# Optimization experiments

Measured on AMD Instinct MI355X. Metric: run time of the kernel, lower is better.

The kernel has to match this reference:

```python
import jax, jax.numpy as jnp
import numpy as np

N_NODES = 20000
N_EDGES = 640000
D = 128            # node feature dim
NUM_HEADS = 4      # = num_irreps of edge_sh (lmax=3, 0e+1o+2e+3o)
HEAD_DIM = D // NUM_HEADS
IR_DIMS = np.array([1, 3, 5, 7])  # dims of each irrep; sum = 16
AVG_NUM_NEIGHBORS = 32.0


def setup_inputs() -> dict:
    key = jax.random.key(0)
    ks = jax.random.split(key, 20)
    inp = {
        "edge_sh": jax.random.normal(ks[0], (N_EDGES, int(IR_DIMS.sum())), jnp.float32),
        "node_feats": jax.random.normal(ks[1], (N_NODES, D), jnp.float32),
        "edge_feats": jax.random.normal(ks[2], (N_EDGES, 64), jnp.float32),
        "chi_scalar": jax.random.normal(ks[3], (N_EDGES, 64), jnp.float32),
        "cutoffs": jax.random.uniform(ks[4], (N_EDGES,), jnp.float32),
        "senders": jax.random.randint(ks[5], (N_EDGES,), 0, N_NODES),
        "receivers": jax.random.randint(ks[6], (N_EDGES,), 0, N_NODES),
        # radial MLP: 64 -> 128 -> 128 (silu between)
        "W_rad1": jax.random.normal(ks[7], (64, 128), jnp.float32) / np.sqrt(64),
        "b_rad1": jnp.zeros((128,), jnp.float32),
        "W_rad2": jax.random.normal(ks[8], (128, 128), jnp.float32) / np.sqrt(128),
        "b_rad2": jnp.zeros((128,), jnp.float32),
        # spherical-scalar MLP: 64 -> 128 -> 128
        "W_sph1": jax.random.normal(ks[9], (64, 128), jnp.float32) / np.sqrt(64),
        "b_sph1": jnp.zeros((128,), jnp.float32),
        "W_sph2": jax.random.normal(ks[10], (128, 128), jnp.float32) / np.sqrt(128),
        "b_sph2": jnp.zeros((128,), jnp.float32),
        # Q/K projections, no bias
        "Wq": jax.random.normal(ks[11], (D, D), jnp.float32) / np.sqrt(D),
        "Wk": jax.random.normal(ks[12], (D, D), jnp.float32) / np.sqrt(D),
    }
    return inp


def reference(edge_sh, node_feats, edge_feats, chi_scalar, cutoffs, senders,
              receivers, W_rad1, b_rad1, W_rad2, b_rad2, W_sph1, b_sph1,
              W_sph2, b_sph2, Wq, Wk):
    silu = jax.nn.silu
    # edge filter: radial MLP + spherical-scalar MLP
    w = silu(edge_feats @ W_rad1 + b_rad1) @ W_rad2 + b_rad2      # [E, D]
    w = w + (silu(chi_scalar @ W_sph1 + b_sph1) @ W_sph2 + b_sph2)
    w = w.reshape(-1, NUM_HEADS, HEAD_DIM)                        # [E, H, hd]
    # gathered queries/keys
    q = (node_feats @ Wq).reshape(-1, NUM_HEADS, HEAD_DIM)[receivers]
    k = (node_feats @ Wk).reshape(-1, NUM_HEADS, HEAD_DIM)[senders]
    # filter-scaled attention: per-edge, per-head scalar
    alpha = (q * w * k).sum(axis=-1) * (1.0 / np.sqrt(HEAD_DIM))  # [E, H]
    alpha = alpha * cutoffs[:, None]
    # aligned_mul: broadcast per-irrep weight over each irrep's dim (mul=1)
    y = jnp.repeat(alpha, IR_DIMS, axis=-1)                       # [E, 16]
    msg = edge_sh * y
    # scatter_sum into receivers
    chi = jax.ops.segment_sum(msg, receivers, num_segments=N_NODES)
    return chi / AVG_NUM_NEIGHBORS
```

## Files before the change

### kernel.cpp

```cpp
#include <hip/hip_runtime.h>
#include <cmath>

#define NNODES 20000
#define NEDGES 640000
#define DDIM   128
#define TN     16
#define BE     64

typedef __attribute__((ext_vector_type(8))) short bf16x8;
typedef __attribute__((ext_vector_type(4))) float f32x4;
typedef __attribute__((ext_vector_type(4))) unsigned short us4;

__device__ __forceinline__ unsigned short f2bf(float x) {
    union { float f; unsigned u; } v; v.f = x;
    unsigned r = v.u + 0x7FFFu + ((v.u >> 16) & 1u);
    return (unsigned short)(r >> 16);
}
__device__ __forceinline__ float bf2f(unsigned short h) {
    union { unsigned u; float f; } v; v.u = ((unsigned)h) << 16; return v.f;
}

__global__ void pack_weights(const float* __restrict__ W, unsigned short* __restrict__ dst)
{
    const int f  = blockIdx.x;
    const int kt = f >> 3, nt = f & 7;
    const int t  = threadIdx.x;
#pragma unroll
    for (int ii = 0; ii < 2; ii++) {
        const int idx  = t * 2 + ii;
        const int lane = idx >> 3, i = idx & 7;
        const int k = kt * 32 + (lane >> 4) * 8 + i;
        const int n = nt * 16 + (lane & 15);
        dst[f * 512 + idx] = f2bf(W[k * 128 + n]);
    }
}

__global__ __launch_bounds__(256) void qk_proj_kernel(
    const float* __restrict__ nf, const float* __restrict__ Wq,
    const float* __restrict__ Wk, float* __restrict__ qbuf,
    float* __restrict__ kbuf)
{
    __shared__ float s_nf[TN * DDIM];
    const int t  = threadIdx.x;
    const int n0 = blockIdx.x * TN;
    {
        const float4* src = (const float4*)(nf + (size_t)n0 * DDIM);
        float4* dst = (float4*)s_nf;
        for (int i = t; i < TN * DDIM / 4; i += 256) dst[i] = src[i];
    }
    __syncthreads();

    const int j = t & 127;
    const float* W = (t < 128) ? Wq : Wk;
    float acc[TN];
#pragma unroll
    for (int n = 0; n < TN; n++) acc[n] = 0.f;

    for (int k = 0; k < DDIM; k += 4) {
        const float w0 = W[(k + 0) * DDIM + j];
        const float w1 = W[(k + 1) * DDIM + j];
        const float w2 = W[(k + 2) * DDIM + j];
        const float w3 = W[(k + 3) * DDIM + j];
#pragma unroll
        for (int n = 0; n < TN; n++) {
            const float4 f = *(const float4*)&s_nf[n * DDIM + k];
            acc[n] = fmaf(f.w, w3, fmaf(f.z, w2, fmaf(f.y, w1, fmaf(f.x, w0, acc[n]))));
        }
    }
    float* outp = (t < 128) ? qbuf : kbuf;
    for (int n = 0; n < TN; n++) outp[(size_t)(n0 + n) * DDIM + j] = acc[n];
}

__global__ __launch_bounds__(256) void edge_kernel(
    const float* __restrict__ edge_sh, const float* __restrict__ cutoffs,
    const int* __restrict__ senders, const int* __restrict__ receivers,
    const float* __restrict__ edge_feats, const float* __restrict__ chi_scalar,
    const unsigned short* __restrict__ w1r, const unsigned short* __restrict__ w1s,
    const unsigned short* __restrict__ w2r, const unsigned short* __restrict__ w2s,
    const float* __restrict__ b_rad1, const float* __restrict__ b_sph1,
    const float* __restrict__ b_rad2, const float* __restrict__ b_sph2,
    const float* __restrict__ qbuf, const float* __restrict__ kbuf,
    float* __restrict__ out)
{
    __shared__ unsigned short s_a[2 * 64 * 64];
    __shared__ unsigned short s_h[64 * 128];
    __shared__ unsigned short s_p[64 * 128];
    __shared__ float s_alpha[64][4];

    char* pa = (char*)s_a;
    char* ph = (char*)s_h;
    char* pp = (char*)s_p;

    const int t  = threadIdx.x;
    const int w  = t >> 6;
    const int l  = t & 63;
    const int eb = blockIdx.x * BE;

#pragma unroll
    for (int ii = 0; ii < 8; ii++) {
        const int e  = w * 16 + ii * 2 + (l >> 5);
        const int eg = eb + e;
        const int r  = receivers[eg];
        const int s  = senders[eg];
        const int c4 = l & 31;
        const float4 qv = *(const float4*)(qbuf + (size_t)r * 128 + c4 * 4);
        const float4 kv = *(const float4*)(kbuf + (size_t)s * 128 + c4 * 4);
        us4 pv = { f2bf(qv.x * kv.x), f2bf(qv.y * kv.y),
                   f2bf(qv.z * kv.z), f2bf(qv.w * kv.w) };
        *(us4*)(pp + ((e * 256 + c4 * 8) ^ ((e & 7) << 4))) = pv;
    }

#pragma unroll
    for (int ii = 0; ii < 4; ii++) {
        const int idx = t + ii * 256;
        const int r   = idx >> 4;
        const int c4  = idx & 15;
        const float4 a = *(const float4*)(edge_feats + (size_t)(eb + r) * 64 + c4 * 4);
        const float4 b = *(const float4*)(chi_scalar + (size_t)(eb + r) * 64 + c4 * 4);
        us4 av = { f2bf(a.x), f2bf(a.y), f2bf(a.z), f2bf(a.w) };
        us4 bv = { f2bf(b.x), f2bf(b.y), f2bf(b.z), f2bf(b.w) };
        const int off = (r * 128 + c4 * 8) ^ ((r & 7) << 4);
        *(us4*)(pa + off)        = av;
        *(us4*)(pa + 8192 + off) = bv;
    }
    __syncthreads();

    f32x4 acc2[2][4];
#pragma unroll
    for (int ct = 0; ct < 2; ct++)
#pragma unroll
        for (int et = 0; et < 4; et++)
            acc2[ct][et] = (f32x4){0.f, 0.f, 0.f, 0.f};

    for (int path = 0; path < 2; path++) {
        const unsigned short* W1p = path ? w1s : w1r;
        const unsigned short* W2p = path ? w2s : w2r;
        const float* b1p = path ? b_sph1 : b_rad1;
        const char*  ab  = pa + path * 8192;

        f32x4 acc1[2][4];
#pragma unroll
        for (int ht = 0; ht < 2; ht++)
#pragma unroll
            for (int et = 0; et < 4; et++)
                acc1[ht][et] = (f32x4){0.f, 0.f, 0.f, 0.f};

#pragma unroll
        for (int kt = 0; kt < 2; kt++) {
            bf16x8 bfrag[4];
#pragma unroll
            for (int et = 0; et < 4; et++) {
                const int e = et * 16 + (l & 15);
                const int k = kt * 32 + (l >> 4) * 8;
                bfrag[et] = *(const bf16x8*)(ab + ((e * 128 + k * 2) ^ ((e & 7) << 4)));
            }
#pragma unroll
            for (int ht = 0; ht < 2; ht++) {
                const int f = kt * 8 + (w * 2 + ht);
                const bf16x8 afrag = *(const bf16x8*)(W1p + (size_t)f * 512 + l * 8);
#pragma unroll
                for (int et = 0; et < 4; et++)
                    acc1[ht][et] = __builtin_amdgcn_mfma_f32_16x16x32_bf16(
                        afrag, bfrag[et], acc1[ht][et], 0, 0, 0);
            }
        }

#pragma unroll
        for (int ht = 0; ht < 2; ht++) {
            const int hid0 = w * 32 + ht * 16 + (l >> 4) * 4;
            const float4 bv = *(const float4*)(b1p + hid0);
#pragma unroll
            for (int et = 0; et < 4; et++) {
                const int e = et * 16 + (l & 15);
                us4 hv;
#pragma unroll
                for (int r = 0; r < 4; r++) {
                    const float v = acc1[ht][et][r] + ((const float*)&bv)[r];
                    const float s = v / (1.0f + __expf(-v));
                    hv[r] = f2bf(s);
                }
                *(us4*)(ph + ((e * 256 + hid0 * 2) ^ ((e & 7) << 4))) = hv;
            }
        }
        __syncthreads();

#pragma unroll
        for (int kt = 0; kt < 4; kt++) {
            bf16x8 hfrag[4];
#pragma unroll
            for (int et = 0; et < 4; et++) {
                const int e = et * 16 + (l & 15);
                const int k = kt * 32 + (l >> 4) * 8;
                hfrag[et] = *(const bf16x8*)(ph + ((e * 256 + k * 2) ^ ((e & 7) << 4)));
            }
#pragma unroll
            for (int ct = 0; ct < 2; ct++) {
                const int f = kt * 8 + (w * 2 + ct);
                const bf16x8 afrag = *(const bf16x8*)(W2p + (size_t)f * 512 + l * 8);
#pragma unroll
                for (int et = 0; et < 4; et++)
                    acc2[ct][et] = __builtin_amdgcn_mfma_f32_16x16x32_bf16(
                        afrag, hfrag[et], acc2[ct][et], 0, 0, 0);
            }
        }
        __syncthreads();
    }

    {
        float vsum[4] = {0.f, 0.f, 0.f, 0.f};
#pragma unroll
        for (int ct = 0; ct < 2; ct++) {
            const int c0 = w * 32 + ct * 16 + (l >> 4) * 4;
            const float4 br = *(const float4*)(b_rad2 + c0);
            const float4 bs = *(const float4*)(b_sph2 + c0);
#pragma unroll
            for (int et = 0; et < 4; et++) {
                const int e = et * 16 + (l & 15);
                const us4 pv = *(const us4*)(pp + ((e * 256 + c0 * 2) ^ ((e & 7) << 4)));
#pragma unroll
                for (int r = 0; r < 4; r++) {
                    const float wv = acc2[ct][et][r] + ((const float*)&br)[r]
                                                    + ((const float*)&bs)[r];
                    vsum[et] = fmaf(bf2f(pv[r]), wv, vsum[et]);
                }
            }
        }
#pragma unroll
        for (int et = 0; et < 4; et++) {
            float v = vsum[et];
            v += __shfl_xor(v, 16, 64);
            v += __shfl_xor(v, 32, 64);
            if (l < 16) {
                const int e = et * 16 + l;
                s_alpha[e][w] = v * cutoffs[eb + e] * 0.005524271728019903f;
            }
        }
    }
    __syncthreads();

    {
        const int e   = t >> 2;
        const int c0q = t & 3;
        const int eg  = eb + e;
        const int r   = receivers[eg];
        const float4 sh = *(const float4*)(edge_sh + (size_t)eg * 16 + c0q * 4);
#pragma unroll
        for (int j = 0; j < 4; j++) {
            const int comp = c0q * 4 + j;
            const int head = (comp == 0) ? 0 : (comp < 4) ? 1 : (comp < 9) ? 2 : 3;
            const float msg = ((const float*)&sh)[j] * s_alpha[e][head];
            atomicAdd(&out[(size_t)r * 16 + comp], msg);
        }
    }
}

extern "C" void kernel_launch(void* const* d_in, const int* in_sizes, int n_in,
                              void* d_out, int out_size, void* d_ws, size_t ws_size,
                              hipStream_t stream)
{
    const float* edge_sh    = (const float*)d_in[0];
    const float* node_feats = (const float*)d_in[1];
    const float* edge_feats = (const float*)d_in[2];
    const float* chi_scalar = (const float*)d_in[3];
    const float* cutoffs    = (const float*)d_in[4];
    const int*   senders    = (const int*)d_in[5];
    const int*   receivers  = (const int*)d_in[6];
    const float* W_rad1 = (const float*)d_in[7];
    const float* b_rad1 = (const float*)d_in[8];
    const float* W_rad2 = (const float*)d_in[9];
    const float* b_rad2 = (const float*)d_in[10];
    const float* W_sph1 = (const float*)d_in[11];
    const float* b_sph1 = (const float*)d_in[12];
    const float* W_sph2 = (const float*)d_in[13];
    const float* b_sph2 = (const float*)d_in[14];
    const float* Wq     = (const float*)d_in[15];
    const float* Wk     = (const float*)d_in[16];

    float* out  = (float*)d_out;
    float* qbuf = (float*)d_ws;
    float* kbuf = qbuf + (size_t)NNODES * DDIM;
    unsigned short* pk = (unsigned short*)(kbuf + (size_t)NNODES * DDIM);
    unsigned short* w1r = pk;
    unsigned short* w1s = w1r + 16 * 512;
    unsigned short* w2r = w1s + 16 * 512;
    unsigned short* w2s = w2r + 32 * 512;

    hipMemsetAsync(out, 0, (size_t)out_size * sizeof(float), stream);

    pack_weights<<<16, 256, 0, stream>>>(W_rad1, w1r);
    pack_weights<<<16, 256, 0, stream>>>(W_sph1, w1s);
    pack_weights<<<32, 256, 0, stream>>>(W_rad2, w2r);
    pack_weights<<<32, 256, 0, stream>>>(W_sph2, w2s);

    qk_proj_kernel<<<NNODES / TN, 256, 0, stream>>>(node_feats, Wq, Wk, qbuf, kbuf);

    edge_kernel<<<NEDGES / BE, 256, 0, stream>>>(
        edge_sh, cutoffs, senders, receivers, edge_feats, chi_scalar,
        w1r, w1s, w2r, w2s, b_rad1, b_sph1, b_rad2, b_sph2,
        qbuf, kbuf, out);
}
```

Baseline: 311.0 us.

## Gather q/k in epilogue, drop product smem and alpha stage, pack bf16 conversions

Removes the up-front q*k gather into shared memory. q and k are now loaded directly in the MFMA epilogue in fp32, aligned with the accumulator layout. The per-head alpha no longer goes through shared memory: each wave's lanes issue atomics only for their own head's irrep components, which removes a barrier and the s_p/s_alpha LDS. Also uses v_cvt_pk_bf16_f32 for packed conversion, rcp instead of divide in SiLU, launch_bounds occupancy hint of 4, and skips the final loop barrier. The trade-off is that atomics are serialized per lane (only 16 lanes active per wave) and the gathers are scattered later in the kernel.

```diff
diff --git a/kernel.cpp b/kernel.cpp
--- a/kernel.cpp
+++ b/kernel.cpp
@@ -9,15 +9,17 @@
 
 typedef __attribute__((ext_vector_type(8))) short bf16x8;
 typedef __attribute__((ext_vector_type(4))) float f32x4;
-typedef __attribute__((ext_vector_type(4))) unsigned short us4;
 
 __device__ __forceinline__ unsigned short f2bf(float x) {
     union { float f; unsigned u; } v; v.f = x;
     unsigned r = v.u + 0x7FFFu + ((v.u >> 16) & 1u);
     return (unsigned short)(r >> 16);
 }
-__device__ __forceinline__ float bf2f(unsigned short h) {
-    union { unsigned u; float f; } v; v.u = ((unsigned)h) << 16; return v.f;
+
+__device__ __forceinline__ unsigned cvtpk(float lo, float hi) {
+    unsigned r;
+    asm("v_cvt_pk_bf16_f32 %0, %1, %2" : "=v"(r) : "v"(lo), "v"(hi));
+    return r;
 }
 
 __global__ void pack_weights(const float* __restrict__ W, unsigned short* __restrict__ dst)
@@ -71,7 +73,7 @@
     for (int n = 0; n < TN; n++) outp[(size_t)(n0 + n) * DDIM + j] = acc[n];
 }
 
-__global__ __launch_bounds__(256) void edge_kernel(
+__global__ __launch_bounds__(256, 4) void edge_kernel(
     const float* __restrict__ edge_sh, const float* __restrict__ cutoffs,
     const int* __restrict__ senders, const int* __restrict__ receivers,
     const float* __restrict__ edge_feats, const float* __restrict__ chi_scalar,
@@ -84,31 +86,13 @@
 {
     __shared__ unsigned short s_a[2 * 64 * 64];
     __shared__ unsigned short s_h[64 * 128];
-    __shared__ unsigned short s_p[64 * 128];
-    __shared__ float s_alpha[64][4];
-
     char* pa = (char*)s_a;
     char* ph = (char*)s_h;
-    char* pp = (char*)s_p;
 
     const int t  = threadIdx.x;
     const int w  = t >> 6;
     const int l  = t & 63;
     const int eb = blockIdx.x * BE;
-
-#pragma unroll
-    for (int ii = 0; ii < 8; ii++) {
-        const int e  = w * 16 + ii * 2 + (l >> 5);
-        const int eg = eb + e;
-        const int r  = receivers[eg];
-        const int s  = senders[eg];
-        const int c4 = l & 31;
-        const float4 qv = *(const float4*)(qbuf + (size_t)r * 128 + c4 * 4);
-        const float4 kv = *(const float4*)(kbuf + (size_t)s * 128 + c4 * 4);
-        us4 pv = { f2bf(qv.x * kv.x), f2bf(qv.y * kv.y),
-                   f2bf(qv.z * kv.z), f2bf(qv.w * kv.w) };
-        *(us4*)(pp + ((e * 256 + c4 * 8) ^ ((e & 7) << 4))) = pv;
-    }
 
 #pragma unroll
     for (int ii = 0; ii < 4; ii++) {
@@ -117,11 +101,11 @@
         const int c4  = idx & 15;
         const float4 a = *(const float4*)(edge_feats + (size_t)(eb + r) * 64 + c4 * 4);
         const float4 b = *(const float4*)(chi_scalar + (size_t)(eb + r) * 64 + c4 * 4);
-        us4 av = { f2bf(a.x), f2bf(a.y), f2bf(a.z), f2bf(a.w) };
-        us4 bv = { f2bf(b.x), f2bf(b.y), f2bf(b.z), f2bf(b.w) };
+        const uint2 av = { cvtpk(a.x, a.y), cvtpk(a.z, a.w) };
+        const uint2 bv = { cvtpk(b.x, b.y), cvtpk(b.z, b.w) };
         const int off = (r * 128 + c4 * 8) ^ ((r & 7) << 4);
-        *(us4*)(pa + off)        = av;
-        *(us4*)(pa + 8192 + off) = bv;
+        *(uint2*)(pa + off)        = av;
+        *(uint2*)(pa + 8192 + off) = bv;
     }
     __syncthreads();
 
@@ -169,17 +153,18 @@
         for (int ht = 0; ht < 2; ht++) {
             const int hid0 = w * 32 + ht * 16 + (l >> 4) * 4;
             const float4 bv = *(const float4*)(b1p + hid0);
+            const float* bvf = (const float*)&bv;
 #pragma unroll
             for (int et = 0; et < 4; et++) {
                 const int e = et * 16 + (l & 15);
-                us4 hv;
+                float s[4];
 #pragma unroll
                 for (int r = 0; r < 4; r++) {
-                    const float v = acc1[ht][et][r] + ((const float*)&bv)[r];
-                    const float s = v / (1.0f + __expf(-v));
-                    hv[r] = f2bf(s);
+                    const float v = acc1[ht][et][r] + bvf[r];
+                    s[r] = v * __builtin_amdgcn_rcpf(1.0f + __expf(-v));
                 }
-                *(us4*)(ph + ((e * 256 + hid0 * 2) ^ ((e & 7) << 4))) = hv;
+                const uint2 hv = { cvtpk(s[0], s[1]), cvtpk(s[2], s[3]) };
+                *(uint2*)(ph + ((e * 256 + hid0 * 2) ^ ((e & 7) << 4))) = hv;
             }
         }
         __syncthreads();
@@ -203,53 +188,52 @@
                         afrag, hfrag[et], acc2[ct][et], 0, 0, 0);
             }
         }
-        __syncthreads();
-    }
-
-    {
-        float vsum[4] = {0.f, 0.f, 0.f, 0.f};
+        if (path == 0) __syncthreads();
+    }
+
+    float alpha[4];
+#pragma unroll
+    for (int et = 0; et < 4; et++) {
+        const int e  = et * 16 + (l & 15);
+        const int eg = eb + e;
+        const int rn = receivers[eg];
+        const int sn = senders[eg];
+        float vsum = 0.f;
 #pragma unroll
         for (int ct = 0; ct < 2; ct++) {
             const int c0 = w * 32 + ct * 16 + (l >> 4) * 4;
+            const float4 qv = *(const float4*)(qbuf + (size_t)rn * 128 + c0);
+            const float4 kv = *(const float4*)(kbuf + (size_t)sn * 128 + c0);
             const float4 br = *(const float4*)(b_rad2 + c0);
             const float4 bs = *(const float4*)(b_sph2 + c0);
-#pragma unroll
-            for (int et = 0; et < 4; et++) {
-                const int e = et * 16 + (l & 15);
-                const us4 pv = *(const us4*)(pp + ((e * 256 + c0 * 2) ^ ((e & 7) << 4)));
-#pragma unroll
-                for (int r = 0; r < 4; r++) {
-                    const float wv = acc2[ct][et][r] + ((const float*)&br)[r]
-                                                    + ((const float*)&bs)[r];
-                    vsum[et] = fmaf(bf2f(pv[r]), wv, vsum[et]);
-                }
-            }
-        }
+            const float* qf = (const float*)&qv;
+            const float* kf = (const float*)&kv;
+            const float* brf = (const float*)&br;
+            const float* bsf = (const float*)&bs;
+#pragma unroll
+            for (int r = 0; r < 4; r++) {
+                const float wv = acc2[ct][et][r] + brf[r] + bsf[r];
+                vsum = fmaf(qf[r] * kf[r], wv, vsum);
+            }
+        }
+        vsum += __shfl_xor(vsum, 16, 64);
+        vsum += __shfl_xor(vsum, 32, 64);
+        alpha[et] = vsum * 0.005524271728019903f;
+    }
+
+    if (l < 16) {
+        const int cstart = (w == 0) ? 0 : (w == 1) ? 1 : (w == 2) ? 4 : 9;
+        const int ccnt   = 2 * w + 1;
 #pragma unroll
         for (int et = 0; et < 4; et++) {
-            float v = vsum[et];
-            v += __shfl_xor(v, 16, 64);
-            v += __shfl_xor(v, 32, 64);
-            if (l < 16) {
-                const int e = et * 16 + l;
-                s_alpha[e][w] = v * cutoffs[eb + e] * 0.005524271728019903f;
-            }
-        }
-    }
-    __syncthreads();
-
-    {
-        const int e   = t >> 2;
-        const int c0q = t & 3;
-        const int eg  = eb + e;
-        const int r   = receivers[eg];
-        const float4 sh = *(const float4*)(edge_sh + (size_t)eg * 16 + c0q * 4);
-#pragma unroll
-        for (int j = 0; j < 4; j++) {
-            const int comp = c0q * 4 + j;
-            const int head = (comp == 0) ? 0 : (comp < 4) ? 1 : (comp < 9) ? 2 : 3;
-            const float msg = ((const float*)&sh)[j] * s_alpha[e][head];
-            atomicAdd(&out[(size_t)r * 16 + comp], msg);
+            const int e  = et * 16 + l;
+            const int eg = eb + e;
+            const int rn = receivers[eg];
+            const float a = alpha[et] * cutoffs[eg];
+            const float* shp = edge_sh + (size_t)eg * 16 + cstart;
+            float* outp = out + (size_t)rn * 16 + cstart;
+            for (int c = 0; c < ccnt; c++)
+                atomicAdd(&outp[c], shp[c] * a);
         }
     }
 }
@@ -279,8 +263,7 @@
     float* out  = (float*)d_out;
     float* qbuf = (float*)d_ws;
     float* kbuf = qbuf + (size_t)NNODES * DDIM;
-    unsigned short* pk = (unsigned short*)(kbuf + (size_t)NNODES * DDIM);
-    unsigned short* w1r = pk;
+    unsigned short* w1r = (unsigned short*)(kbuf + (size_t)NNODES * DDIM);
     unsigned short* w1s = w1r + 16 * 512;
     unsigned short* w2r = w1s + 16 * 512;
     unsigned short* w2s = w2r + 32 * 512;
```

New measurement: 653.8 us. 110% more time.
